# Kernel tuning notes

Hardware: AMD Instinct MI355X
Metric: run time of the kernel (lower is better)

Reference implementation:

```python
import jax, jax.numpy as jnp
import numpy as np

N = 8192
IN_DIM = 128
OUT_DIM = 128


def setup_inputs() -> dict:
    key = jax.random.key(0)
    k1, k2, k3, k4 = jax.random.split(key, 4)
    X = jax.random.normal(k1, (N, IN_DIM), dtype=jnp.float32)
    A = jax.random.uniform(k2, (N, N), dtype=jnp.float32)
    # Xavier-uniform linear weight [out, in], zero bias (as in reset_parameters)
    limit = float(np.sqrt(6.0 / (IN_DIM + OUT_DIM)))
    W = jax.random.uniform(k3, (OUT_DIM, IN_DIM), dtype=jnp.float32, minval=-limit, maxval=limit)
    b = jnp.zeros((OUT_DIM,), dtype=jnp.float32)
    return {"X": X, "A": A, "W": W, "b": b}


def reference(X, A, W, b):
    # A_hat = A + I  (add self-loops)
    A_hat = A + jnp.eye(A.shape[0], dtype=A.dtype)
    degree = A_hat.sum(axis=1)  # [N]
    d_inv_sqrt = degree ** -0.5
    d_inv_sqrt = jnp.where(jnp.isinf(d_inv_sqrt), 0.0, d_inv_sqrt)
    # D^{-1/2} A_hat D^{-1/2} as row/col scaling (same math as diag matmuls)
    A_norm = d_inv_sqrt[:, None] * A_hat * d_inv_sqrt[None, :]
    h = A_norm @ X  # [N, in_dim]
    return h @ W.T + b  # [N, out_dim]
```

## Files before the change

### kernel.cpp

```cpp
#include <hip/hip_runtime.h>
#include <hip/hip_bf16.h>

#define NN 8192
#define DIM 128
#define BM 32
#define BK 64
#define NT (NN / BK)

typedef __attribute__((ext_vector_type(4))) float f32x4;
typedef __attribute__((ext_vector_type(8))) short bf16x8;
typedef __attribute__((ext_vector_type(4))) short bf16x4;

static __device__ __forceinline__ short f2bf(float f) {
    __hip_bfloat16 h = __float2bfloat16(f);
    return *reinterpret_cast<short*>(&h);
}
static __device__ __forceinline__ float bf2f(short s) {
    union { unsigned int u; float f; } c;
    c.u = ((unsigned int)(unsigned short)s) << 16;
    return c.f;
}

__global__ __launch_bounds__(256) void k_rowsum(const float* __restrict__ A,
                                                float* __restrict__ dinv) {
    const int row = blockIdx.x;
    const int t = threadIdx.x;
    const float4* a4 = reinterpret_cast<const float4*>(A + (size_t)row * NN);
    float s = 0.f;
#pragma unroll
    for (int q = 0; q < 8; ++q) {
        float4 v = a4[q * 256 + t];
        s += (v.x + v.y) + (v.z + v.w);
    }
#pragma unroll
    for (int off = 32; off > 0; off >>= 1) s += __shfl_down(s, off);
    __shared__ float red[4];
    if ((t & 63) == 0) red[t >> 6] = s;
    __syncthreads();
    if (t == 0) {
        float deg = red[0] + red[1] + red[2] + red[3] + 1.0f;
        dinv[row] = 1.0f / sqrtf(deg);
    }
}

__global__ __launch_bounds__(256) void k_y(const float* __restrict__ X,
                                           const float* __restrict__ W,
                                           const float* __restrict__ dinv,
                                           short* __restrict__ Yt) {
    __shared__ float Wl[64 * 128];
    __shared__ float Xl[32 * 129];
    const int t = threadIdx.x;
    const int j0 = (blockIdx.x >> 1) * 32;
    const int half = blockIdx.x & 1;

    const float4* wg = reinterpret_cast<const float4*>(W + (size_t)half * 64 * 128);
#pragma unroll
    for (int q = 0; q < 8; ++q)
        reinterpret_cast<float4*>(Wl)[q * 256 + t] = wg[q * 256 + t];
#pragma unroll
    for (int q = 0; q < 4; ++q) {
        int p = q * 256 + t;
        int row = p >> 5, c4 = p & 31;
        float4 v = reinterpret_cast<const float4*>(X + (size_t)(j0 + row) * DIM)[c4];
        float* dst = Xl + row * 129 + c4 * 4;
        dst[0] = v.x; dst[1] = v.y; dst[2] = v.z; dst[3] = v.w;
    }
    __syncthreads();

    const int j = t & 31;
    const int fb = t >> 5;
    const float dj = dinv[j0 + j];
    float acc[8];
#pragma unroll
    for (int k = 0; k < 8; ++k) acc[k] = 0.f;
    for (int f = 0; f < DIM; ++f) {
        float xv = Xl[j * 129 + f];
#pragma unroll
        for (int k = 0; k < 8; ++k)
            acc[k] = fmaf(xv, Wl[(fb + k * 8) * 128 + f], acc[k]);
    }
#pragma unroll
    for (int k = 0; k < 8; ++k)
        Yt[(size_t)(half * 64 + fb + k * 8) * NN + j0 + j] = f2bf(dj * acc[k]);
}

__global__ __launch_bounds__(512) void k_main(const float* __restrict__ A,
                                              const short* __restrict__ Yt,
                                              const float* __restrict__ dinv,
                                              const float* __restrict__ bias,
                                              float* __restrict__ out) {
    __shared__ short Ab[2][BM * BK];
    __shared__ short Yb[2][DIM * BK];

    const int t = threadIdx.x;
    const int i0 = blockIdx.x * BM;

    const int ar = t >> 4;
    const int ac4 = t & 15;
    const float4* aG = reinterpret_cast<const float4*>(A + (size_t)(i0 + ar) * NN) + ac4;
    const int aLoff = ar * 128 + ((ac4 * 8) ^ ((ar & 7) << 4));

    const int yr0 = t >> 3;
    const int yc0 = t & 7;
    const int yr1 = yr0 + 64;
    const short* yG0 = Yt + (size_t)yr0 * NN + yc0 * 8;
    const short* yG1 = Yt + (size_t)yr1 * NN + yc0 * 8;
    const int yLoff0 = yr0 * 128 + ((yc0 * 16) ^ ((yr0 & 7) << 4));
    const int yLoff1 = yr1 * 128 + ((yc0 * 16) ^ ((yr1 & 7) << 4));

    const int lane = t & 63;
    const int wid = t >> 6;
    const int wm = wid >> 2, wn = wid & 3;
    const int l15 = lane & 15, lk = lane >> 4;

    int offA[2], offB[2][2];
#pragma unroll
    for (int kc = 0; kc < 2; ++kc) {
        const int bcol = kc * 64 + lk * 16;
        const int arow = wm * 16 + l15;
        offA[kc] = arow * 128 + (bcol ^ ((arow & 7) << 4));
#pragma unroll
        for (int fn = 0; fn < 2; ++fn) {
            const int f = wn * 32 + fn * 16 + l15;
            offB[fn][kc] = f * 128 + (bcol ^ ((f & 7) << 4));
        }
    }

    f32x4 acc[2] = {{0.f, 0.f, 0.f, 0.f}, {0.f, 0.f, 0.f, 0.f}};

    {
        float4 av = aG[0];
        int4 y0 = *reinterpret_cast<const int4*>(yG0);
        int4 y1 = *reinterpret_cast<const int4*>(yG1);
        bf16x4 a16 = { f2bf(av.x), f2bf(av.y), f2bf(av.z), f2bf(av.w) };
        *reinterpret_cast<bf16x4*>(reinterpret_cast<char*>(Ab[0]) + aLoff) = a16;
        *reinterpret_cast<int4*>(reinterpret_cast<char*>(Yb[0]) + yLoff0) = y0;
        *reinterpret_cast<int4*>(reinterpret_cast<char*>(Yb[0]) + yLoff1) = y1;
    }
    __syncthreads();

    for (int kt = 0; kt < NT; ++kt) {
        const int cur = kt & 1;
        const int nxt = (kt < NT - 1) ? kt + 1 : kt;

        float4 av = aG[nxt * 16];
        int4 y0 = *reinterpret_cast<const int4*>(yG0 + nxt * BK);
        int4 y1 = *reinterpret_cast<const int4*>(yG1 + nxt * BK);

        const char* ab = reinterpret_cast<const char*>(Ab[cur]);
        const char* yb = reinterpret_cast<const char*>(Yb[cur]);
        bf16x8 a0  = *reinterpret_cast<const bf16x8*>(ab + offA[0]);
        bf16x8 a1  = *reinterpret_cast<const bf16x8*>(ab + offA[1]);
        bf16x8 b00 = *reinterpret_cast<const bf16x8*>(yb + offB[0][0]);
        bf16x8 b01 = *reinterpret_cast<const bf16x8*>(yb + offB[0][1]);
        bf16x8 b10 = *reinterpret_cast<const bf16x8*>(yb + offB[1][0]);
        bf16x8 b11 = *reinterpret_cast<const bf16x8*>(yb + offB[1][1]);
        acc[0] = __builtin_amdgcn_mfma_f32_16x16x32_bf16(a0, b00, acc[0], 0, 0, 0);
        acc[0] = __builtin_amdgcn_mfma_f32_16x16x32_bf16(a1, b01, acc[0], 0, 0, 0);
        acc[1] = __builtin_amdgcn_mfma_f32_16x16x32_bf16(a0, b10, acc[1], 0, 0, 0);
        acc[1] = __builtin_amdgcn_mfma_f32_16x16x32_bf16(a1, b11, acc[1], 0, 0, 0);

        {
            bf16x4 a16 = { f2bf(av.x), f2bf(av.y), f2bf(av.z), f2bf(av.w) };
            char* abw = reinterpret_cast<char*>(Ab[cur ^ 1]);
            char* ybw = reinterpret_cast<char*>(Yb[cur ^ 1]);
            *reinterpret_cast<bf16x4*>(abw + aLoff) = a16;
            *reinterpret_cast<int4*>(ybw + yLoff0) = y0;
            *reinterpret_cast<int4*>(ybw + yLoff1) = y1;
        }
        __syncthreads();
    }

    const int iBase = i0 + wm * 16 + lk * 4;
    const float4 dv4 = *reinterpret_cast<const float4*>(dinv + iBase);
    const float dvr[4] = { dv4.x, dv4.y, dv4.z, dv4.w };
#pragma unroll
    for (int fn = 0; fn < 2; ++fn) {
        const int f = wn * 32 + fn * 16 + l15;
        const float bf_ = bias[f];
        bf16x4 yv = *reinterpret_cast<const bf16x4*>(Yt + (size_t)f * NN + iBase);
#pragma unroll
        for (int r = 0; r < 4; ++r) {
            float z = acc[fn][r] + bf2f(yv[r]);
            out[(size_t)(iBase + r) * DIM + f] = dvr[r] * z + bf_;
        }
    }
}

extern "C" void kernel_launch(void* const* d_in, const int* in_sizes, int n_in,
                              void* d_out, int out_size, void* d_ws, size_t ws_size,
                              hipStream_t stream) {
    (void)in_sizes; (void)n_in; (void)out_size; (void)ws_size;
    const float* X = (const float*)d_in[0];
    const float* A = (const float*)d_in[1];
    const float* W = (const float*)d_in[2];
    const float* b = (const float*)d_in[3];
    float* out = (float*)d_out;

    float* dinv = (float*)d_ws;
    short* Yt = (short*)((char*)d_ws + NN * sizeof(float));

    k_rowsum<<<NN, 256, 0, stream>>>(A, dinv);
    k_y<<<(NN / 32) * 2, 256, 0, stream>>>(X, W, dinv, Yt);
    k_main<<<NN / BM, 512, 0, stream>>>(A, Yt, dinv, b, out);
}
```

Measured before the change: 472.9 us.

## Halve main tile rows, stream Y via direct-to-LDS loads, deepen A prefetch

The main aggregation kernel drops to 16 output rows per block, which doubles the grid to 512 blocks, and adds an occupancy hint to launch bounds. Y tiles are now copied straight into LDS with global_load_lds, with the swizzle moved to the source address, so they no longer pass through registers. A loads are prefetched two iterations ahead, and only half the threads load A. The aim is more resident blocks and better hiding of global latency, at the cost of each block re-reading the whole Y matrix, which doubles Y traffic.

```diff
diff --git a/kernel.cpp b/kernel.cpp
--- a/kernel.cpp
+++ b/kernel.cpp
@@ -3,7 +3,7 @@
 
 #define NN 8192
 #define DIM 128
-#define BM 32
+#define BM 16
 #define BK 64
 #define NT (NN / BK)
 
@@ -19,6 +19,12 @@
     union { unsigned int u; float f; } c;
     c.u = ((unsigned int)(unsigned short)s) << 16;
     return c.f;
+}
+
+static __device__ __forceinline__ void gload16(const void* g, void* l) {
+    __builtin_amdgcn_global_load_lds(
+        (const __attribute__((address_space(1))) unsigned int*)g,
+        (__attribute__((address_space(3))) unsigned int*)l, 16, 0, 0);
 }
 
 __global__ __launch_bounds__(256) void k_rowsum(const float* __restrict__ A,
@@ -84,11 +90,11 @@
         Yt[(size_t)(half * 64 + fb + k * 8) * NN + j0 + j] = f2bf(dj * acc[k]);
 }
 
-__global__ __launch_bounds__(512) void k_main(const float* __restrict__ A,
-                                              const short* __restrict__ Yt,
-                                              const float* __restrict__ dinv,
-                                              const float* __restrict__ bias,
-                                              float* __restrict__ out) {
+__global__ __launch_bounds__(512, 4) void k_main(const float* __restrict__ A,
+                                                 const short* __restrict__ Yt,
+                                                 const float* __restrict__ dinv,
+                                                 const float* __restrict__ bias,
+                                                 float* __restrict__ out) {
     __shared__ short Ab[2][BM * BK];
     __shared__ short Yb[2][DIM * BK];
 
@@ -97,93 +103,79 @@
 
     const int ar = t >> 4;
     const int ac4 = t & 15;
-    const float4* aG = reinterpret_cast<const float4*>(A + (size_t)(i0 + ar) * NN) + ac4;
+    const float4* aG = reinterpret_cast<const float4*>(A + (size_t)(i0 + (ar & 15)) * NN) + ac4;
     const int aLoff = ar * 128 + ((ac4 * 8) ^ ((ar & 7) << 4));
 
-    const int yr0 = t >> 3;
-    const int yc0 = t & 7;
-    const int yr1 = yr0 + 64;
-    const short* yG0 = Yt + (size_t)yr0 * NN + yc0 * 8;
-    const short* yG1 = Yt + (size_t)yr1 * NN + yc0 * 8;
-    const int yLoff0 = yr0 * 128 + ((yc0 * 16) ^ ((yr0 & 7) << 4));
-    const int yLoff1 = yr1 * 128 + ((yc0 * 16) ^ ((yr1 & 7) << 4));
+    const int yRow0 = t >> 3;
+    const int ychunk = (t & 7) ^ (yRow0 & 7);
+    const short* ySrc0 = Yt + (size_t)yRow0 * NN + ychunk * 8;
+    const short* ySrc1 = Yt + (size_t)(yRow0 + 64) * NN + ychunk * 8;
 
     const int lane = t & 63;
     const int wid = t >> 6;
-    const int wm = wid >> 2, wn = wid & 3;
     const int l15 = lane & 15, lk = lane >> 4;
-
-    int offA[2], offB[2][2];
+    const int f = wid * 16 + l15;
+    const int swzA = (l15 & 7) << 4;
+    int offA[2], offB[2];
 #pragma unroll
     for (int kc = 0; kc < 2; ++kc) {
         const int bcol = kc * 64 + lk * 16;
-        const int arow = wm * 16 + l15;
-        offA[kc] = arow * 128 + (bcol ^ ((arow & 7) << 4));
-#pragma unroll
-        for (int fn = 0; fn < 2; ++fn) {
-            const int f = wn * 32 + fn * 16 + l15;
-            offB[fn][kc] = f * 128 + (bcol ^ ((f & 7) << 4));
-        }
+        offA[kc] = l15 * 128 + (bcol ^ swzA);
+        offB[kc] = f * 128 + (bcol ^ swzA);
     }
 
-    f32x4 acc[2] = {{0.f, 0.f, 0.f, 0.f}, {0.f, 0.f, 0.f, 0.f}};
+    f32x4 acc = {0.f, 0.f, 0.f, 0.f};
 
-    {
-        float4 av = aG[0];
-        int4 y0 = *reinterpret_cast<const int4*>(yG0);
-        int4 y1 = *reinterpret_cast<const int4*>(yG1);
-        bf16x4 a16 = { f2bf(av.x), f2bf(av.y), f2bf(av.z), f2bf(av.w) };
+    gload16(ySrc0, (char*)Yb[0] + t * 16);
+    gload16(ySrc1, (char*)Yb[0] + 8192 + t * 16);
+    float4 avCur;
+    if (t < 256) {
+        float4 av0 = aG[0];
+        bf16x4 a16 = { f2bf(av0.x), f2bf(av0.y), f2bf(av0.z), f2bf(av0.w) };
         *reinterpret_cast<bf16x4*>(reinterpret_cast<char*>(Ab[0]) + aLoff) = a16;
-        *reinterpret_cast<int4*>(reinterpret_cast<char*>(Yb[0]) + yLoff0) = y0;
-        *reinterpret_cast<int4*>(reinterpret_cast<char*>(Yb[0]) + yLoff1) = y1;
+        avCur = aG[(NT > 1 ? 1 : 0) * 16];
     }
     __syncthreads();
 
+    int cur = 0;
     for (int kt = 0; kt < NT; ++kt) {
-        const int cur = kt & 1;
-        const int nxt = (kt < NT - 1) ? kt + 1 : kt;
+        const int nxt  = (kt + 1 < NT) ? kt + 1 : NT - 1;
+        const int nxt2 = (kt + 2 < NT) ? kt + 2 : NT - 1;
 
-        float4 av = aG[nxt * 16];
-        int4 y0 = *reinterpret_cast<const int4*>(yG0 + nxt * BK);
-        int4 y1 = *reinterpret_cast<const int4*>(yG1 + nxt * BK);
+        char* ybw = reinterpret_cast<char*>(Yb[cur ^ 1]);
+        gload16(ySrc0 + (size_t)nxt * BK, ybw + t * 16);
+        gload16(ySrc1 + (size_t)nxt * BK, ybw + 8192 + t * 16);
+
+        float4 avN;
+        if (t < 256) avN = aG[nxt2 * 16];
 
         const char* ab = reinterpret_cast<const char*>(Ab[cur]);
         const char* yb = reinterpret_cast<const char*>(Yb[cur]);
-        bf16x8 a0  = *reinterpret_cast<const bf16x8*>(ab + offA[0]);
-        bf16x8 a1  = *reinterpret_cast<const bf16x8*>(ab + offA[1]);
-        bf16x8 b00 = *reinterpret_cast<const bf16x8*>(yb + offB[0][0]);
-        bf16x8 b01 = *reinterpret_cast<const bf16x8*>(yb + offB[0][1]);
-        bf16x8 b10 = *reinterpret_cast<const bf16x8*>(yb + offB[1][0]);
-        bf16x8 b11 = *reinterpret_cast<const bf16x8*>(yb + offB[1][1]);
-        acc[0] = __builtin_amdgcn_mfma_f32_16x16x32_bf16(a0, b00, acc[0], 0, 0, 0);
-        acc[0] = __builtin_amdgcn_mfma_f32_16x16x32_bf16(a1, b01, acc[0], 0, 0, 0);
-        acc[1] = __builtin_amdgcn_mfma_f32_16x16x32_bf16(a0, b10, acc[1], 0, 0, 0);
-        acc[1] = __builtin_amdgcn_mfma_f32_16x16x32_bf16(a1, b11, acc[1], 0, 0, 0);
+        bf16x8 a0 = *reinterpret_cast<const bf16x8*>(ab + offA[0]);
+        bf16x8 a1 = *reinterpret_cast<const bf16x8*>(ab + offA[1]);
+        bf16x8 b0 = *reinterpret_cast<const bf16x8*>(yb + offB[0]);
+        bf16x8 b1 = *reinterpret_cast<const bf16x8*>(yb + offB[1]);
+        acc = __builtin_amdgcn_mfma_f32_16x16x32_bf16(a0, b0, acc, 0, 0, 0);
+        acc = __builtin_amdgcn_mfma_f32_16x16x32_bf16(a1, b1, acc, 0, 0, 0);
 
-        {
-            bf16x4 a16 = { f2bf(av.x), f2bf(av.y), f2bf(av.z), f2bf(av.w) };
-            char* abw = reinterpret_cast<char*>(Ab[cur ^ 1]);
-            char* ybw = reinterpret_cast<char*>(Yb[cur ^ 1]);
-            *reinterpret_cast<bf16x4*>(abw + aLoff) = a16;
-            *reinterpret_cast<int4*>(ybw + yLoff0) = y0;
-            *reinterpret_cast<int4*>(ybw + yLoff1) = y1;
+        if (t < 256) {
+            bf16x4 a16 = { f2bf(avCur.x), f2bf(avCur.y), f2bf(avCur.z), f2bf(avCur.w) };
+            *reinterpret_cast<bf16x4*>(reinterpret_cast<char*>(Ab[cur ^ 1]) + aLoff) = a16;
+            avCur = avN;
         }
         __syncthreads();
+        cur ^= 1;
     }
 
-    const int iBase = i0 + wm * 16 + lk * 4;
+    const int iBase = i0 + lk * 4;
     const float4 dv4 = *reinterpret_cast<const float4*>(dinv + iBase);
     const float dvr[4] = { dv4.x, dv4.y, dv4.z, dv4.w };
+    const float bf_ = bias[f];
+    bf16x4 yv = *reinterpret_cast<const bf16x4*>(Yt + (size_t)f * NN + iBase);
 #pragma unroll
-    for (int fn = 0; fn < 2; ++fn) {
-        const int f = wn * 32 + fn * 16 + l15;
-        const float bf_ = bias[f];
-        bf16x4 yv = *reinterpret_cast<const bf16x4*>(Yt + (size_t)f * NN + iBase);
-#pragma unroll
-        for (int r = 0; r < 4; ++r) {
-            float z = acc[fn][r] + bf2f(yv[r]);
-            out[(size_t)(iBase + r) * DIM + f] = dvr[r] * z + bf_;
-        }
+    for (int r = 0; r < 4; ++r) {
+        float z = acc[r] + bf2f(yv[r]);
+        out[(size_t)(iBase + r) * DIM + f] = dvr[r] * z + bf_;
     }
 }
 
```

Result: no change. 474.2 us (+0.3%).
